# Performance work log

Hardware: AMD Instinct MI355X
Metric: run time of the kernel (lower is better)

## Reference

```python
import jax, jax.numpy as jnp
import numpy as np

IN_FEATURES = 512
ACTION_DIM = 32
TRIL_DIM = ACTION_DIM * (ACTION_DIM + 1) // 2  # 528
BATCH = 65536
# Row-major lower-triangular indices; matches torch boolean-mask assignment order.
_ROWS, _COLS = np.tril_indices(ACTION_DIM)


def setup_inputs() -> dict:
    key = jax.random.key(0)
    k1, k2, k3, k4, k5 = jax.random.split(key, 5)
    logits = jax.random.normal(k1, (BATCH, IN_FEATURES), dtype=jnp.float32)
    best_action = jax.random.normal(k2, (BATCH, ACTION_DIM), dtype=jnp.float32)
    actions = jax.random.normal(k3, (BATCH, ACTION_DIM), dtype=jnp.float32)
    W = jax.random.normal(k4, (TRIL_DIM, IN_FEATURES), dtype=jnp.float32) * 0.02
    b = jax.random.normal(k5, (TRIL_DIM,), dtype=jnp.float32) * 0.02
    return {"logits": logits, "best_action": best_action, "actions": actions, "W": W, "b": b}


def reference(logits, best_action, actions, W, b):
    # Linear: [B, in_features] -> [B, tril_dim]
    flat_trils = logits @ W.T + b
    B = logits.shape[0]
    n = ACTION_DIM
    # Scatter flat vector into lower-triangular slots (row-major order).
    mats = jnp.zeros((B, n, n), dtype=flat_trils.dtype).at[:, _ROWS, _COLS].set(flat_trils)
    diag = jnp.eye(n, dtype=flat_trils.dtype)
    # Square the diagonal entries, keep off-diagonal entries as-is.
    tril = mats * mats * diag + (1.0 - diag) * mats
    action_diff = actions - best_action  # [B, n]
    vec = jnp.einsum('bij,bj->bi', tril, action_diff)  # [B, n]
    advantage = -0.5 * jnp.sum(vec * vec, axis=-1, keepdims=True)  # [B, 1]
    return advantage
```

## Files before the change

### kernel.cpp

```cpp
#include <hip/hip_runtime.h>
#include <hip/hip_bf16.h>


typedef __attribute__((ext_vector_type(8))) __bf16 bf16x8;
typedef __attribute__((ext_vector_type(4))) float f32x4;

#define AS1 __attribute__((address_space(1)))
#define AS3 __attribute__((address_space(3)))

__device__ __forceinline__ unsigned short f2b(float x) {
  unsigned u = __builtin_bit_cast(unsigned, x);
  u += 0x7fffu + ((u >> 16) & 1u);
  return (unsigned short)(u >> 16);
}
__device__ __forceinline__ float b2f(unsigned short h) {
  unsigned u = ((unsigned)h) << 16;
  return __builtin_bit_cast(float, u);
}

#define NFRAG 34
#define WK_BYTES (NFRAG * 1024)
#define ATILE_BYTES (128 * 32 * 4)
#define BUF_BYTES (WK_BYTES + ATILE_BYTES)
#define A_IN_BUF WK_BYTES
#define FLAT_STRIDE 532
#define DIFF_OFF (128 * FLAT_STRIDE * 2)
#define SMEM_BYTES (DIFF_OFF + 128 * 32 * 4)

__global__ void prep_wp(const float* __restrict__ W, unsigned short* __restrict__ WP) {
  int t = blockIdx.x * 256 + threadIdx.x;
  int lane = t & 63;
  int u = t >> 6;
  int nf = u % NFRAG;
  int k16 = u / NFRAG;
  int n = nf * 16 + (lane & 15);
  int k0 = k16 * 32 + (lane >> 4) * 8;
  unsigned short h[8];
  if (n < 528) {
    const float* src = W + (size_t)n * 512 + k0;
#pragma unroll
    for (int j = 0; j < 8; ++j) h[j] = f2b(src[j]);
  } else {
#pragma unroll
    for (int j = 0; j < 8; ++j) h[j] = 0;
  }
  uint4 p;
  p.x = (unsigned)h[0] | ((unsigned)h[1] << 16);
  p.y = (unsigned)h[2] | ((unsigned)h[3] << 16);
  p.z = (unsigned)h[4] | ((unsigned)h[5] << 16);
  p.w = (unsigned)h[6] | ((unsigned)h[7] << 16);
  *(uint4*)(WP + (size_t)t * 8) = p;
}

__global__ void __launch_bounds__(512, 2)
adv_kernel(const float* __restrict__ logits,
           const float* __restrict__ best,
           const float* __restrict__ actions,
           const float* __restrict__ bvec,
           const unsigned short* __restrict__ WP,
           float* __restrict__ out) {
  extern __shared__ char smem[];
  const int tid = threadIdx.x;
  const int l   = tid & 63;
  const int wid = tid >> 6;
  const int lr  = l & 15;
  const int lg  = l >> 4;
  const int wc  = wid & 3;
  const int wrbase = (wid >> 2) * 64;
  const int start = wc * 8 + (wc > 0 ? 1 : 0);
  const int brow = blockIdx.x * 128;

  f32x4 acc[4][9];
  {
    f32x4 zero = {0.f, 0.f, 0.f, 0.f};
#pragma unroll
    for (int m = 0; m < 4; ++m)
#pragma unroll
      for (int n = 0; n < 9; ++n) acc[m][n] = zero;
  }

  int aoff[4][2];
#pragma unroll
  for (int m = 0; m < 4; ++m)
#pragma unroll
    for (int h = 0; h < 2; ++h)
      aoff[m][h] = (wrbase + m * 16 + lr) * 128 +
                   ((lg * 32 + h * 16) ^ ((lr & 7) << 4));
  int boff[9];
#pragma unroll
  for (int n = 0; n < 9; ++n) boff[n] = (start + n) * 1024 + l * 16;

#define STAGE_A(dst, ks)                                                        \
  {                                                                             \
    char* dA = (dst) + A_IN_BUF;                                                \
    _Pragma("unroll")                                                           \
    for (int p = 0; p < 2; ++p) {                                               \
      int c = p * 512 + tid;                                                    \
      int row = c >> 3, hh = c & 7;                                             \
      const float* g = logits + (size_t)(brow + row) * 512 + (ks) * 32 +        \
                       ((hh ^ (row & 7)) << 2);                                 \
      __builtin_amdgcn_global_load_lds((AS1 unsigned int*)g,                    \
          (AS3 unsigned int*)(dA + (p * 512 + wid * 64) * 16), 16, 0, 0);       \
    }                                                                           \
  }
#define STAGE_W(dst, ks)                                                        \
  {                                                                             \
    const char* sW = (const char*)WP + (size_t)(ks) * WK_BYTES;                 \
    _Pragma("unroll")                                                           \
    for (int q = 0; q < 4; ++q) {                                               \
      int off = (q * 8 + wid) * 1024;                                           \
      __builtin_amdgcn_global_load_lds((AS1 unsigned int*)(sW + off + l * 16),  \
          (AS3 unsigned int*)((dst) + off), 16, 0, 0);                          \
    }                                                                           \
    if (wid < 2) {                                                              \
      int off = (32 + wid) * 1024;                                              \
      __builtin_amdgcn_global_load_lds((AS1 unsigned int*)(sW + off + l * 16),  \
          (AS3 unsigned int*)((dst) + off), 16, 0, 0);                          \
    }                                                                           \
  }

  STAGE_A(smem, 0)
  STAGE_W(smem, 0)
  __syncthreads();

  for (int t = 0; t < 16; ++t) {
    char* buf = smem + (t & 1) * BUF_BYTES;
    if (t < 15) {
      char* nb = smem + ((t & 1) ^ 1) * BUF_BYTES;
      STAGE_A(nb, t + 1)
      STAGE_W(nb, t + 1)
    }
    bf16x8 a[4];
#pragma unroll
    for (int m = 0; m < 4; ++m) {
      f32x4 x0 = *(const f32x4*)(buf + A_IN_BUF + aoff[m][0]);
      f32x4 x1 = *(const f32x4*)(buf + A_IN_BUF + aoff[m][1]);
      bf16x8 af;
      af[0] = (__bf16)x0[0]; af[1] = (__bf16)x0[1];
      af[2] = (__bf16)x0[2]; af[3] = (__bf16)x0[3];
      af[4] = (__bf16)x1[0]; af[5] = (__bf16)x1[1];
      af[6] = (__bf16)x1[2]; af[7] = (__bf16)x1[3];
      a[m] = af;
    }
#pragma unroll
    for (int n = 0; n < 9; ++n) {
      bf16x8 bfr = *(const bf16x8*)(buf + boff[n]);
#pragma unroll
      for (int m = 0; m < 4; ++m)
        acc[m][n] = __builtin_amdgcn_mfma_f32_16x16x32_bf16(a[m], bfr, acc[m][n], 0, 0, 0);
    }
    if (t < 15) __syncthreads();
  }
  __syncthreads();

  unsigned short* fl = (unsigned short*)smem;
#pragma unroll
  for (int n = 0; n < 9; ++n) {
    int nf = start + n;
    if (nf >= 33) continue;
    int f = nf * 16 + lr;
    float bb = bvec[f];
#pragma unroll
    for (int m = 0; m < 4; ++m)
#pragma unroll
      for (int r = 0; r < 4; ++r) {
        int row = wrbase + m * 16 + lg * 4 + r;
        fl[row * FLAT_STRIDE + f] = f2b(acc[m][n][r] + bb);
      }
  }
  {
    float* dl = (float*)(smem + DIFF_OFF);
    int row = tid >> 2;
    int j0  = (tid & 3) << 3;
    const float* ap = actions + (size_t)(brow + row) * 32 + j0;
    const float* bp = best    + (size_t)(brow + row) * 32 + j0;
    float4 a0 = *(const float4*)(ap);
    float4 a1 = *(const float4*)(ap + 4);
    float4 b0 = *(const float4*)(bp);
    float4 b1 = *(const float4*)(bp + 4);
    float d[8] = {a0.x - b0.x, a0.y - b0.y, a0.z - b0.z, a0.w - b0.w,
                  a1.x - b1.x, a1.y - b1.y, a1.z - b1.z, a1.w - b1.w};
    int rs = row & 31;
#pragma unroll
    for (int q = 0; q < 8; ++q)
      dl[row * 32 + ((j0 + q) ^ rs)] = d[q];
  }
  __syncthreads();

  {
    int it  = tid & 3;
    int row = tid >> 2;
    const unsigned short* flr = fl + row * FLAT_STRIDE;
    const float* dlr = (const float*)(smem + DIFF_OFF) + row * 32;
    int rs = row & 31;
    float ssum = 0.f;
#pragma unroll
    for (int ii = 0; ii < 8; ++ii) {
      int i = it + ii * 4;
      int tri = (i * (i + 1)) >> 1;
      float vec = 0.f;
      for (int j = 0; j < i; ++j)
        vec += b2f(flr[tri + j]) * dlr[j ^ rs];
      float dv = b2f(flr[tri + i]);
      vec += dv * dv * dlr[i ^ rs];
      ssum += vec * vec;
    }
    ssum += __shfl_xor(ssum, 1);
    ssum += __shfl_xor(ssum, 2);
    if (it == 0) out[brow + row] = -0.5f * ssum;
  }
}

extern "C" void kernel_launch(void* const* d_in, const int* in_sizes, int n_in,
                              void* d_out, int out_size, void* d_ws, size_t ws_size,
                              hipStream_t stream) {
  const float* logits  = (const float*)d_in[0];
  const float* best    = (const float*)d_in[1];
  const float* actions = (const float*)d_in[2];
  const float* W       = (const float*)d_in[3];
  const float* bvec    = (const float*)d_in[4];
  float* out = (float*)d_out;
  unsigned short* WP = (unsigned short*)d_ws;

  hipLaunchKernelGGL(prep_wp, dim3(136), dim3(256), 0, stream, W, WP);
  int M = in_sizes[0] / 512;
  hipLaunchKernelGGL(adv_kernel, dim3(M / 128), dim3(512), SMEM_BYTES, stream,
                     logits, best, actions, bvec, WP, out);
}
```

Baseline: 61.82 us.

## Halve block tile and stage bf16 logits via register prefetch

The block shrinks from 128 rows and 512 threads to 64 rows and 256 threads, so each wave now covers all 64 rows for its own column fragments. Logits are no longer copied to LDS as fp32 by every block. Each thread loads them into registers two k-steps ahead, converts them to bf16 once, and writes them to a small double-buffered LDS tile. This removes the repeated fp32-to-bf16 conversion done by every column wave and shrinks LDS use, allowing more blocks to be resident per CU. In exchange, the W panel is re-read from L2 twice as often per row, and the prefetched values add register pressure.

```diff
diff --git a/kernel.cpp b/kernel.cpp
--- a/kernel.cpp
+++ b/kernel.cpp
@@ -20,12 +20,10 @@
 
 #define NFRAG 34
 #define WK_BYTES (NFRAG * 1024)
-#define ATILE_BYTES (128 * 32 * 4)
-#define BUF_BYTES (WK_BYTES + ATILE_BYTES)
-#define A_IN_BUF WK_BYTES
+#define AOFF (2 * WK_BYTES)
+#define SMEM_BYTES (AOFF + 2 * 4096)
 #define FLAT_STRIDE 532
-#define DIFF_OFF (128 * FLAT_STRIDE * 2)
-#define SMEM_BYTES (DIFF_OFF + 128 * 32 * 4)
+#define DIFF_OFF (64 * FLAT_STRIDE * 2)
 
 __global__ void prep_wp(const float* __restrict__ W, unsigned short* __restrict__ WP) {
   int t = blockIdx.x * 256 + threadIdx.x;
@@ -52,7 +50,7 @@
   *(uint4*)(WP + (size_t)t * 8) = p;
 }
 
-__global__ void __launch_bounds__(512, 2)
+__global__ void __launch_bounds__(256, 2)
 adv_kernel(const float* __restrict__ logits,
            const float* __restrict__ best,
            const float* __restrict__ actions,
@@ -65,10 +63,8 @@
   const int wid = tid >> 6;
   const int lr  = l & 15;
   const int lg  = l >> 4;
-  const int wc  = wid & 3;
-  const int wrbase = (wid >> 2) * 64;
-  const int start = wc * 8 + (wc > 0 ? 1 : 0);
-  const int brow = blockIdx.x * 128;
+  const int start = wid * 8 + (wid > 0 ? 1 : 0);
+  const int brow = blockIdx.x * 64;
 
   f32x4 acc[4][9];
   {
@@ -79,36 +75,14 @@
       for (int n = 0; n < 9; ++n) acc[m][n] = zero;
   }
 
-  int aoff[4][2];
-#pragma unroll
-  for (int m = 0; m < 4; ++m)
-#pragma unroll
-    for (int h = 0; h < 2; ++h)
-      aoff[m][h] = (wrbase + m * 16 + lr) * 128 +
-                   ((lg * 32 + h * 16) ^ ((lr & 7) << 4));
-  int boff[9];
-#pragma unroll
-  for (int n = 0; n < 9; ++n) boff[n] = (start + n) * 1024 + l * 16;
-
-#define STAGE_A(dst, ks)                                                        \
-  {                                                                             \
-    char* dA = (dst) + A_IN_BUF;                                                \
-    _Pragma("unroll")                                                           \
-    for (int p = 0; p < 2; ++p) {                                               \
-      int c = p * 512 + tid;                                                    \
-      int row = c >> 3, hh = c & 7;                                             \
-      const float* g = logits + (size_t)(brow + row) * 512 + (ks) * 32 +        \
-                       ((hh ^ (row & 7)) << 2);                                 \
-      __builtin_amdgcn_global_load_lds((AS1 unsigned int*)g,                    \
-          (AS3 unsigned int*)(dA + (p * 512 + wid * 64) * 16), 16, 0, 0);       \
-    }                                                                           \
-  }
+  const float* agbase = logits + (size_t)(brow + wid * 16 + lr) * 512 + lg * 8;
+
 #define STAGE_W(dst, ks)                                                        \
   {                                                                             \
     const char* sW = (const char*)WP + (size_t)(ks) * WK_BYTES;                 \
     _Pragma("unroll")                                                           \
-    for (int q = 0; q < 4; ++q) {                                               \
-      int off = (q * 8 + wid) * 1024;                                           \
+    for (int q = 0; q < 8; ++q) {                                               \
+      int off = (q * 4 + wid) * 1024;                                           \
       __builtin_amdgcn_global_load_lds((AS1 unsigned int*)(sW + off + l * 16),  \
           (AS3 unsigned int*)((dst) + off), 16, 0, 0);                          \
     }                                                                           \
@@ -119,39 +93,50 @@
     }                                                                           \
   }
 
-  STAGE_A(smem, 0)
+#define LOAD_A(dst, ks)                                                         \
+  {                                                                             \
+    const float* g = agbase + (ks) * 32;                                        \
+    (dst)[0] = *(const float4*)(g);                                             \
+    (dst)[1] = *(const float4*)(g + 4);                                         \
+  }
+
+#define WRITE_A(buf_idx, src)                                                   \
+  {                                                                             \
+    uint4 p;                                                                    \
+    p.x = f2b((src)[0].x) | ((unsigned)f2b((src)[0].y) << 16);                  \
+    p.y = f2b((src)[0].z) | ((unsigned)f2b((src)[0].w) << 16);                  \
+    p.z = f2b((src)[1].x) | ((unsigned)f2b((src)[1].y) << 16);                  \
+    p.w = f2b((src)[1].z) | ((unsigned)f2b((src)[1].w) << 16);                  \
+    *(uint4*)(smem + AOFF + (buf_idx) * 4096 + tid * 16) = p;                   \
+  }
+
+  float4 pf[2][2];
+  LOAD_A(pf[0], 0)
+  LOAD_A(pf[1], 1)
   STAGE_W(smem, 0)
+  WRITE_A(0, pf[0])
   __syncthreads();
 
+#pragma unroll
   for (int t = 0; t < 16; ++t) {
-    char* buf = smem + (t & 1) * BUF_BYTES;
-    if (t < 15) {
-      char* nb = smem + ((t & 1) ^ 1) * BUF_BYTES;
-      STAGE_A(nb, t + 1)
-      STAGE_W(nb, t + 1)
-    }
+    char* wb = smem + (t & 1) * WK_BYTES;
+    const char* ab = smem + AOFF + (t & 1) * 4096;
+    if (t < 15) STAGE_W(smem + ((t + 1) & 1) * WK_BYTES, t + 1)
+    if (t < 14) LOAD_A(pf[t & 1], t + 2)
     bf16x8 a[4];
 #pragma unroll
-    for (int m = 0; m < 4; ++m) {
-      f32x4 x0 = *(const f32x4*)(buf + A_IN_BUF + aoff[m][0]);
-      f32x4 x1 = *(const f32x4*)(buf + A_IN_BUF + aoff[m][1]);
-      bf16x8 af;
-      af[0] = (__bf16)x0[0]; af[1] = (__bf16)x0[1];
-      af[2] = (__bf16)x0[2]; af[3] = (__bf16)x0[3];
-      af[4] = (__bf16)x1[0]; af[5] = (__bf16)x1[1];
-      af[6] = (__bf16)x1[2]; af[7] = (__bf16)x1[3];
-      a[m] = af;
-    }
+    for (int m = 0; m < 4; ++m)
+      a[m] = *(const bf16x8*)(ab + m * 1024 + l * 16);
 #pragma unroll
     for (int n = 0; n < 9; ++n) {
-      bf16x8 bfr = *(const bf16x8*)(buf + boff[n]);
+      bf16x8 bfr = *(const bf16x8*)(wb + (start + n) * 1024 + l * 16);
 #pragma unroll
       for (int m = 0; m < 4; ++m)
         acc[m][n] = __builtin_amdgcn_mfma_f32_16x16x32_bf16(a[m], bfr, acc[m][n], 0, 0, 0);
     }
-    if (t < 15) __syncthreads();
-  }
-  __syncthreads();
+    if (t < 15) WRITE_A((t + 1) & 1, pf[(t + 1) & 1])
+    __syncthreads();
+  }
 
   unsigned short* fl = (unsigned short*)smem;
 #pragma unroll
@@ -164,7 +149,7 @@
     for (int m = 0; m < 4; ++m)
 #pragma unroll
       for (int r = 0; r < 4; ++r) {
-        int row = wrbase + m * 16 + lg * 4 + r;
+        int row = m * 16 + lg * 4 + r;
         fl[row * FLAT_STRIDE + f] = f2b(acc[m][n][r] + bb);
       }
   }
@@ -224,6 +209,6 @@
 
   hipLaunchKernelGGL(prep_wp, dim3(136), dim3(256), 0, stream, W, WP);
   int M = in_sizes[0] / 512;
-  hipLaunchKernelGGL(adv_kernel, dim3(M / 128), dim3(512), SMEM_BYTES, stream,
+  hipLaunchKernelGGL(adv_kernel, dim3(M / 64), dim3(256), SMEM_BYTES, stream,
                      logits, best, actions, bvec, WP, out);
 }
```

After: 95.01 us. 1.54x slower.
